# Kernel tuning notes

Measured on AMD Instinct MI355X. Metric: run time of the kernel, lower is better.

The kernel has to match this reference:

```python
import jax, jax.numpy as jnp
import numpy as np

NUM_NODES = 100000
EMB_DIM = 64
NUM_LAYERS = 3
DROPOUT_P = 0.1
NUM_EDGES = 1200000


def setup_inputs() -> dict:
    key = jax.random.key(0)
    k1, k2 = jax.random.split(key)
    # Xavier-uniform init for the embedding table (as in the torch module)
    limit = (6.0 / (NUM_NODES + EMB_DIM)) ** 0.5
    emb_weight = jax.random.uniform(k1, (NUM_NODES, EMB_DIM), jnp.float32, -limit, limit)
    edge_index = jax.random.randint(k2, (2, NUM_EDGES), 0, NUM_NODES, dtype=jnp.int32)
    return {"emb_weight": emb_weight, "edge_index": edge_index}


def _lightgcn(x, edge_index):
    # Standard LightGCN propagation: x_{l+1} = A_hat x_l with symmetric norm,
    # output = mean over layer embeddings 0..L.
    src, dst = edge_index[0], edge_index[1]
    ones = jnp.ones((edge_index.shape[1],), dtype=x.dtype)
    deg = jax.ops.segment_sum(ones, dst, num_segments=NUM_NODES)
    deg_inv_sqrt = jnp.where(deg > 0, jax.lax.rsqrt(jnp.maximum(deg, 1.0)), 0.0)
    norm = deg_inv_sqrt[src] * deg_inv_sqrt[dst]  # [E]
    out = x
    acc = x
    for _ in range(NUM_LAYERS):
        msg = out[src] * norm[:, None]                       # gather [E, D]
        out = jax.ops.segment_sum(msg, dst, num_segments=NUM_NODES)  # scatter-add [N, D]
        acc = acc + out
    return acc / (NUM_LAYERS + 1)


def _dropout(x, p, key):
    keep = jax.random.bernoulli(key, 1.0 - p, x.shape)
    return jnp.where(keep, x / (1.0 - p), jnp.zeros((), x.dtype))


def reference(emb_weight, edge_index):
    out = _lightgcn(emb_weight, edge_index)
    # Dropout in train mode, fixed key for reproducibility
    return _dropout(out, DROPOUT_P, jax.random.key(42))
```

## Files before the change

kernel.cpp:

```cpp
#include <hip/hip_runtime.h>
#include <math.h>

#define N_NODES 100000
#define EMB 64
#define N_EDGES 1200000
#define N_ELEM (N_NODES * EMB)
#define SCAN_CHUNK 1024
#define SCAN_NBLK ((N_NODES + SCAN_CHUNK - 1) / SCAN_CHUNK)
#define NPART 8
#define PART_SIZE (N_NODES / NPART)
#define SC_GRID 1024
#define SC_TPB 256

__device__ __forceinline__ unsigned rotl32(unsigned v, int r) {
    return (v << r) | (v >> (32 - r));
}

__device__ __forceinline__ void threefry2x32(unsigned k0, unsigned k1,
                                             unsigned c0, unsigned c1,
                                             unsigned& o0, unsigned& o1) {
    const unsigned ks0 = k0;
    const unsigned ks1 = k1;
    const unsigned ks2 = k0 ^ k1 ^ 0x1BD11BDAu;
    unsigned x0 = c0 + ks0;
    unsigned x1 = c1 + ks1;
#define TF_RND(r) { x0 += x1; x1 = rotl32(x1, r); x1 ^= x0; }
    TF_RND(13) TF_RND(15) TF_RND(26) TF_RND(6)
    x0 += ks1; x1 += ks2 + 1u;
    TF_RND(17) TF_RND(29) TF_RND(16) TF_RND(24)
    x0 += ks2; x1 += ks0 + 2u;
    TF_RND(13) TF_RND(15) TF_RND(26) TF_RND(6)
    x0 += ks0; x1 += ks1 + 3u;
    TF_RND(17) TF_RND(29) TF_RND(16) TF_RND(24)
    x0 += ks1; x1 += ks2 + 4u;
    TF_RND(13) TF_RND(15) TF_RND(26) TF_RND(6)
    x0 += ks2; x1 += ks0 + 5u;
#undef TF_RND
    o0 = x0;
    o1 = x1;
}

__device__ __forceinline__ bool drop_keep(unsigned i) {
    unsigned o0, o1;
    threefry2x32(0u, 42u, 0u, i, o0, o1);
    unsigned bits = o0 ^ o1;
    float u = __uint_as_float((bits >> 9) | 0x3f800000u) - 1.0f;
    return u < 0.9f;
}

__global__ void k_hist(const int* __restrict__ dst, int* __restrict__ cnt) {
    int e = blockIdx.x * blockDim.x + threadIdx.x;
    if (e < N_EDGES) atomicAdd(&cnt[dst[e]], 1);
}

__global__ void k_scan1(const int* __restrict__ cnt, int* __restrict__ local,
                        int* __restrict__ bsum, float* __restrict__ dis) {
    __shared__ int wsum[16];
    const int tid = threadIdx.x;
    const int lane = tid & 63;
    const int wid = tid >> 6;
    int i = blockIdx.x * SCAN_CHUNK + tid;
    int v = (i < N_NODES) ? cnt[i] : 0;
    if (i < N_NODES) dis[i] = (v > 0) ? rsqrtf((float)v) : 0.0f;
    int x = v;
#pragma unroll
    for (int off = 1; off < 64; off <<= 1) {
        int t = __shfl_up(x, off, 64);
        if (lane >= off) x += t;
    }
    if (lane == 63) wsum[wid] = x;
    __syncthreads();
    if (wid == 0 && lane < 16) {
        int w = wsum[lane];
#pragma unroll
        for (int off = 1; off < 16; off <<= 1) {
            int t = __shfl_up(w, off, 64);
            if (lane >= off) w += t;
        }
        wsum[lane] = w;
    }
    __syncthreads();
    int wexc = (wid == 0) ? 0 : wsum[wid - 1];
    if (i < N_NODES) local[i] = (x + wexc) - v;
    if (tid == 0) bsum[blockIdx.x] = wsum[15];
}

__global__ void k_scan2(const int* __restrict__ bsum, int* __restrict__ bofs) {
    __shared__ int sh[128];
    int t = threadIdx.x;
    int v = (t < SCAN_NBLK) ? bsum[t] : 0;
    sh[t] = v;
    __syncthreads();
    for (int off = 1; off < 128; off <<= 1) {
        int add = (t >= off) ? sh[t - off] : 0;
        __syncthreads();
        sh[t] += add;
        __syncthreads();
    }
    if (t < SCAN_NBLK) bofs[t] = sh[t] - v;
}

__global__ void k_scan3(int* __restrict__ cursor_local, const int* __restrict__ bofs,
                        int* __restrict__ rowptr) {
    int i = blockIdx.x * SCAN_CHUNK + threadIdx.x;
    if (i < N_NODES) {
        int r = cursor_local[i] + bofs[blockIdx.x];
        rowptr[i] = r;
        cursor_local[i] = r;
    }
    if (i == 0) rowptr[N_NODES] = N_EDGES;
}

__global__ void k_scatter(const int* __restrict__ src, const int* __restrict__ dst,
                          const float* __restrict__ dis, int* __restrict__ cursor,
                          int2* __restrict__ edges) {
    const int p = blockIdx.x & (NPART - 1);
    const int lo = p * PART_SIZE;
    const int hi = lo + PART_SIZE;
    const int stride = (SC_GRID / NPART) * SC_TPB;
    int e = (blockIdx.x >> 3) * SC_TPB + threadIdx.x;
    for (; e < N_EDGES; e += stride) {
        int d = dst[e];
        if (d >= lo && d < hi) {
            int s = src[e];
            int pos = atomicAdd(&cursor[d], 1);
            edges[pos] = make_int2(s, __float_as_int(dis[s] * dis[d]));
        }
    }
}

template <int MODE>
__global__ void k_agg(const int* __restrict__ rowptr, const int2* __restrict__ edges,
                      const float* __restrict__ x, float* __restrict__ y,
                      float* __restrict__ acc) {
    const int gwid = (blockIdx.x * blockDim.x + threadIdx.x) >> 6;
    const int lane = threadIdx.x & 63;
    const int g = lane >> 4;
    const int l16 = lane & 15;
    const int n = (gwid << 2) + g;
    if (n >= N_NODES) return;
    const int begin = rowptr[n];
    const int end = rowptr[n + 1];
    const float* xb = x + (l16 << 2);
    float4 s = make_float4(0.f, 0.f, 0.f, 0.f);
    int j = begin;
    for (; j + 3 < end; j += 4) {
        int2 r0 = edges[j];
        int2 r1 = edges[j + 1];
        int2 r2 = edges[j + 2];
        int2 r3 = edges[j + 3];
        const float4 v0 = *reinterpret_cast<const float4*>(xb + (size_t)r0.x * EMB);
        const float4 v1 = *reinterpret_cast<const float4*>(xb + (size_t)r1.x * EMB);
        const float4 v2 = *reinterpret_cast<const float4*>(xb + (size_t)r2.x * EMB);
        const float4 v3 = *reinterpret_cast<const float4*>(xb + (size_t)r3.x * EMB);
        float n0 = __int_as_float(r0.y), n1 = __int_as_float(r1.y);
        float n2 = __int_as_float(r2.y), n3 = __int_as_float(r3.y);
        s.x += v0.x * n0 + v1.x * n1 + v2.x * n2 + v3.x * n3;
        s.y += v0.y * n0 + v1.y * n1 + v2.y * n2 + v3.y * n3;
        s.z += v0.z * n0 + v1.z * n1 + v2.z * n2 + v3.z * n3;
        s.w += v0.w * n0 + v1.w * n1 + v2.w * n2 + v3.w * n3;
    }
    for (; j < end; ++j) {
        int2 r0 = edges[j];
        float n0 = __int_as_float(r0.y);
        const float4 v0 = *reinterpret_cast<const float4*>(xb + (size_t)r0.x * EMB);
        s.x += v0.x * n0; s.y += v0.y * n0; s.z += v0.z * n0; s.w += v0.w * n0;
    }
    const size_t ridx = (size_t)n * EMB + (l16 << 2);
    if (MODE == 0) {
        *reinterpret_cast<float4*>(y + ridx) = s;
        float4 own = *reinterpret_cast<const float4*>(x + ridx);
        *reinterpret_cast<float4*>(acc + ridx) =
            make_float4(own.x + s.x, own.y + s.y, own.z + s.z, own.w + s.w);
    } else if (MODE == 1) {
        *reinterpret_cast<float4*>(y + ridx) = s;
        float4 a = *reinterpret_cast<const float4*>(acc + ridx);
        *reinterpret_cast<float4*>(acc + ridx) =
            make_float4(a.x + s.x, a.y + s.y, a.z + s.z, a.w + s.w);
    } else {
        float4 a = *reinterpret_cast<const float4*>(acc + ridx);
        float4 t = make_float4(a.x + s.x, a.y + s.y, a.z + s.z, a.w + s.w);
        const float sc = 0.25f / 0.9f;
        unsigned base = (unsigned)ridx;
        float4 o;
        o.x = drop_keep(base + 0u) ? t.x * sc : 0.f;
        o.y = drop_keep(base + 1u) ? t.y * sc : 0.f;
        o.z = drop_keep(base + 2u) ? t.z * sc : 0.f;
        o.w = drop_keep(base + 3u) ? t.w * sc : 0.f;
        *reinterpret_cast<float4*>(acc + ridx) = o;
    }
}

extern "C" void kernel_launch(void* const* d_in, const int* in_sizes, int n_in,
                              void* d_out, int out_size, void* d_ws, size_t ws_size,
                              hipStream_t stream) {
    const float* emb = (const float*)d_in[0];
    const int* eidx = (const int*)d_in[1];
    const int* src = eidx;
    const int* dst = eidx + N_EDGES;
    float* acc = (float*)d_out;

    char* ws = (char*)d_ws;
    int*   cnt     = (int*)(ws + 0);
    int*   cursor  = (int*)(ws + 400000);
    int*   bsum    = (int*)(ws + 800000);
    int*   bofs    = (int*)(ws + 800400);
    int*   rowptr  = (int*)(ws + 800800);
    float* dis     = (float*)(ws + 1200808);
    int2*  edges   = (int2*)(ws + 1600808);
    float* bufA    = (float*)(ws + 11200816);
    float* bufB    = (float*)(ws + 36800816);

    const int BLK = 256;
    const int gE   = (N_EDGES + BLK - 1) / BLK;
    const int gAgg = ((N_NODES + 3) / 4 * 64 + BLK - 1) / BLK;

    hipMemsetAsync(cnt, 0, N_NODES * sizeof(int), stream);
    k_hist<<<gE, BLK, 0, stream>>>(dst, cnt);
    k_scan1<<<SCAN_NBLK, SCAN_CHUNK, 0, stream>>>(cnt, cursor, bsum, dis);
    k_scan2<<<1, 128, 0, stream>>>(bsum, bofs);
    k_scan3<<<SCAN_NBLK, SCAN_CHUNK, 0, stream>>>(cursor, bofs, rowptr);
    k_scatter<<<SC_GRID, SC_TPB, 0, stream>>>(src, dst, dis, cursor, edges);

    k_agg<0><<<gAgg, BLK, 0, stream>>>(rowptr, edges, emb,  bufA, acc);
    k_agg<1><<<gAgg, BLK, 0, stream>>>(rowptr, edges, bufA, bufB, acc);
    k_agg<2><<<gAgg, BLK, 0, stream>>>(rowptr, edges, bufB, nullptr, acc);
}
```

Baseline: 368.4 us.

## Store propagated embeddings in fp16 to halve gather traffic

Adds a conversion kernel that casts the input embedding table to half precision. The three aggregation passes now gather neighbor rows as fp16 and store intermediate layer outputs as fp16, while accumulating in fp32 and keeping the fp32 accumulator and output. This is meant to halve the bytes of the random-access neighbor gathers, which dominate the aggregation cost. In exchange it adds a conversion pass and introduces fp16 rounding error in the intermediate layers.

```diff
diff --git a/kernel.cpp b/kernel.cpp
--- a/kernel.cpp
+++ b/kernel.cpp
@@ -1,4 +1,5 @@
 #include <hip/hip_runtime.h>
+#include <hip/hip_fp16.h>
 #include <math.h>
 
 #define N_NODES 100000
@@ -48,6 +49,21 @@
     return u < 0.9f;
 }
 
+__global__ void k_cvt(const float* __restrict__ in, __half* __restrict__ out) {
+    int base = (blockIdx.x * blockDim.x + threadIdx.x) * 8;
+    if (base >= N_ELEM) return;
+    const float4 f0 = *reinterpret_cast<const float4*>(in + base);
+    const float4 f1 = *reinterpret_cast<const float4*>(in + base + 4);
+    __half2 h0 = __float22half2_rn(make_float2(f0.x, f0.y));
+    __half2 h1 = __float22half2_rn(make_float2(f0.z, f0.w));
+    __half2 h2 = __float22half2_rn(make_float2(f1.x, f1.y));
+    __half2 h3 = __float22half2_rn(make_float2(f1.z, f1.w));
+    uint4 u;
+    u.x = *(unsigned*)&h0; u.y = *(unsigned*)&h1;
+    u.z = *(unsigned*)&h2; u.w = *(unsigned*)&h3;
+    *reinterpret_cast<uint4*>(out + base) = u;
+}
+
 __global__ void k_hist(const int* __restrict__ dst, int* __restrict__ cnt) {
     int e = blockIdx.x * blockDim.x + threadIdx.x;
     if (e < N_EDGES) atomicAdd(&cnt[dst[e]], 1);
@@ -129,10 +145,16 @@
     }
 }
 
+__device__ __forceinline__ float4 h4_to_f4(uint2 u) {
+    __half2 p = *(__half2*)&u.x, q = *(__half2*)&u.y;
+    float2 a = __half22float2(p), b = __half22float2(q);
+    return make_float4(a.x, a.y, b.x, b.y);
+}
+
 template <int MODE>
 __global__ void k_agg(const int* __restrict__ rowptr, const int2* __restrict__ edges,
-                      const float* __restrict__ x, float* __restrict__ y,
-                      float* __restrict__ acc) {
+                      const __half* __restrict__ x, __half* __restrict__ y,
+                      const float* __restrict__ own, float* __restrict__ acc) {
     const int gwid = (blockIdx.x * blockDim.x + threadIdx.x) >> 6;
     const int lane = threadIdx.x & 63;
     const int g = lane >> 4;
@@ -141,7 +163,7 @@
     if (n >= N_NODES) return;
     const int begin = rowptr[n];
     const int end = rowptr[n + 1];
-    const float* xb = x + (l16 << 2);
+    const __half* xb = x + (l16 << 2);
     float4 s = make_float4(0.f, 0.f, 0.f, 0.f);
     int j = begin;
     for (; j + 3 < end; j += 4) {
@@ -149,10 +171,11 @@
         int2 r1 = edges[j + 1];
         int2 r2 = edges[j + 2];
         int2 r3 = edges[j + 3];
-        const float4 v0 = *reinterpret_cast<const float4*>(xb + (size_t)r0.x * EMB);
-        const float4 v1 = *reinterpret_cast<const float4*>(xb + (size_t)r1.x * EMB);
-        const float4 v2 = *reinterpret_cast<const float4*>(xb + (size_t)r2.x * EMB);
-        const float4 v3 = *reinterpret_cast<const float4*>(xb + (size_t)r3.x * EMB);
+        uint2 u0 = *reinterpret_cast<const uint2*>(xb + (size_t)r0.x * EMB);
+        uint2 u1 = *reinterpret_cast<const uint2*>(xb + (size_t)r1.x * EMB);
+        uint2 u2 = *reinterpret_cast<const uint2*>(xb + (size_t)r2.x * EMB);
+        uint2 u3 = *reinterpret_cast<const uint2*>(xb + (size_t)r3.x * EMB);
+        float4 v0 = h4_to_f4(u0), v1 = h4_to_f4(u1), v2 = h4_to_f4(u2), v3 = h4_to_f4(u3);
         float n0 = __int_as_float(r0.y), n1 = __int_as_float(r1.y);
         float n2 = __int_as_float(r2.y), n3 = __int_as_float(r3.y);
         s.x += v0.x * n0 + v1.x * n1 + v2.x * n2 + v3.x * n3;
@@ -163,20 +186,25 @@
     for (; j < end; ++j) {
         int2 r0 = edges[j];
         float n0 = __int_as_float(r0.y);
-        const float4 v0 = *reinterpret_cast<const float4*>(xb + (size_t)r0.x * EMB);
+        float4 v0 = h4_to_f4(*reinterpret_cast<const uint2*>(xb + (size_t)r0.x * EMB));
         s.x += v0.x * n0; s.y += v0.y * n0; s.z += v0.z * n0; s.w += v0.w * n0;
     }
     const size_t ridx = (size_t)n * EMB + (l16 << 2);
-    if (MODE == 0) {
-        *reinterpret_cast<float4*>(y + ridx) = s;
-        float4 own = *reinterpret_cast<const float4*>(x + ridx);
-        *reinterpret_cast<float4*>(acc + ridx) =
-            make_float4(own.x + s.x, own.y + s.y, own.z + s.z, own.w + s.w);
-    } else if (MODE == 1) {
-        *reinterpret_cast<float4*>(y + ridx) = s;
-        float4 a = *reinterpret_cast<const float4*>(acc + ridx);
-        *reinterpret_cast<float4*>(acc + ridx) =
-            make_float4(a.x + s.x, a.y + s.y, a.z + s.z, a.w + s.w);
+    if (MODE == 0 || MODE == 1) {
+        __half2 h0 = __float22half2_rn(make_float2(s.x, s.y));
+        __half2 h1 = __float22half2_rn(make_float2(s.z, s.w));
+        uint2 u;
+        u.x = *(unsigned*)&h0; u.y = *(unsigned*)&h1;
+        *reinterpret_cast<uint2*>(y + ridx) = u;
+        if (MODE == 0) {
+            float4 o = *reinterpret_cast<const float4*>(own + ridx);
+            *reinterpret_cast<float4*>(acc + ridx) =
+                make_float4(o.x + s.x, o.y + s.y, o.z + s.z, o.w + s.w);
+        } else {
+            float4 a = *reinterpret_cast<const float4*>(acc + ridx);
+            *reinterpret_cast<float4*>(acc + ridx) =
+                make_float4(a.x + s.x, a.y + s.y, a.z + s.z, a.w + s.w);
+        }
     } else {
         float4 a = *reinterpret_cast<const float4*>(acc + ridx);
         float4 t = make_float4(a.x + s.x, a.y + s.y, a.z + s.z, a.w + s.w);
@@ -201,19 +229,23 @@
     float* acc = (float*)d_out;
 
     char* ws = (char*)d_ws;
-    int*   cnt     = (int*)(ws + 0);
-    int*   cursor  = (int*)(ws + 400000);
-    int*   bsum    = (int*)(ws + 800000);
-    int*   bofs    = (int*)(ws + 800400);
-    int*   rowptr  = (int*)(ws + 800800);
-    float* dis     = (float*)(ws + 1200808);
-    int2*  edges   = (int2*)(ws + 1600808);
-    float* bufA    = (float*)(ws + 11200816);
-    float* bufB    = (float*)(ws + 36800816);
+    int*    cnt     = (int*)(ws + 0);
+    int*    cursor  = (int*)(ws + 400000);
+    int*    bsum    = (int*)(ws + 800000);
+    int*    bofs    = (int*)(ws + 800400);
+    int*    rowptr  = (int*)(ws + 800800);
+    float*  dis     = (float*)(ws + 1200808);
+    int2*   edges   = (int2*)(ws + 1600808);
+    __half* embh    = (__half*)(ws + 11200816);
+    __half* bufAh   = (__half*)(ws + 24000832);
+    __half* bufBh   = (__half*)(ws + 36800832);
 
     const int BLK = 256;
     const int gE   = (N_EDGES + BLK - 1) / BLK;
+    const int gCvt = (N_ELEM / 8 + BLK - 1) / BLK;
     const int gAgg = ((N_NODES + 3) / 4 * 64 + BLK - 1) / BLK;
+
+    k_cvt<<<gCvt, BLK, 0, stream>>>(emb, embh);
 
     hipMemsetAsync(cnt, 0, N_NODES * sizeof(int), stream);
     k_hist<<<gE, BLK, 0, stream>>>(dst, cnt);
@@ -222,7 +254,7 @@
     k_scan3<<<SCAN_NBLK, SCAN_CHUNK, 0, stream>>>(cursor, bofs, rowptr);
     k_scatter<<<SC_GRID, SC_TPB, 0, stream>>>(src, dst, dis, cursor, edges);
 
-    k_agg<0><<<gAgg, BLK, 0, stream>>>(rowptr, edges, emb,  bufA, acc);
-    k_agg<1><<<gAgg, BLK, 0, stream>>>(rowptr, edges, bufA, bufB, acc);
-    k_agg<2><<<gAgg, BLK, 0, stream>>>(rowptr, edges, bufB, nullptr, acc);
-}
+    k_agg<0><<<gAgg, BLK, 0, stream>>>(rowptr, edges, embh,  bufAh, emb, acc);
+    k_agg<1><<<gAgg, BLK, 0, stream>>>(rowptr, edges, bufAh, bufBh, nullptr, acc);
+    k_agg<2><<<gAgg, BLK, 0, stream>>>(rowptr, edges, bufBh, nullptr, nullptr, acc);
+}
```

After: 324.8 us. 1.13x faster.
